# Kernel tuning notes

Hardware: AMD Instinct MI355X
Metric: run time of the kernel (lower is better)

Reference implementation:

```python
import jax, jax.numpy as jnp
import numpy as np

STRIDE = 1
PADDING = 1

def setup_inputs() -> dict:
    key = jax.random.key(0)
    k1, k2, k3 = jax.random.split(key, 3)
    N, C_in, H, W = 32, 128, 56, 56
    C_out, K = 256, 3
    inputs = jax.random.normal(k1, (N, C_in, H, W), dtype=jnp.float32)
    # trunc_normal(std=0.1) approximated by clipped normal
    filters = jnp.clip(jax.random.normal(k2, (C_out, C_in, K, K), dtype=jnp.float32) * 0.1, -0.2, 0.2)
    bias = jnp.clip(jax.random.normal(k3, (C_out,), dtype=jnp.float32) * 0.1, -0.2, 0.2)
    return {"inputs": inputs, "filters": filters, "bias": bias}

def reference(inputs, filters, bias):
    # Equivalent of the quadruple-loop conv: standard cross-correlation,
    # NCHW input, OIHW filters, stride/padding from module config.
    out = jax.lax.conv_general_dilated(
        inputs, filters,
        window_strides=(STRIDE, STRIDE),
        padding=[(PADDING, PADDING), (PADDING, PADDING)],
        dimension_numbers=("NCHW", "OIHW", "NCHW"),
    )
    out = out + bias[None, :, None, None]
    return out
```

## Files before the change

kernel.cpp:

```cpp
#include <hip/hip_runtime.h>

#define CIN    128
#define HH     56
#define WW_    56
#define NBATCH 32
#define COUT   256
#define KTOT   1152
#define PLANE  3136
#define HP     58
#define BM     128
#define BN     128
#define BK     64

#define WB_OFF   0
#define WB_BYTES (COUT * KTOT * 2)
#define XP_OFF   (1u << 20)
#define XP_BYTES (NBATCH * HP * HP * CIN * 2)

typedef __attribute__((ext_vector_type(8))) short bf16x8;
typedef __attribute__((ext_vector_type(4))) float f32x4;

__device__ __forceinline__ unsigned short f2bf(float f) {
    unsigned int u = __builtin_bit_cast(unsigned int, f);
    u += 0x7fffu + ((u >> 16) & 1u);
    return (unsigned short)(u >> 16);
}

__device__ __forceinline__ void gl_lds16(const void* g, void* l) {
    __builtin_amdgcn_global_load_lds(
        (const __attribute__((address_space(1))) void*)g,
        (__attribute__((address_space(3))) void*)l, 16, 0, 0);
}

__global__ void wprep(const float* __restrict__ w, unsigned short* __restrict__ wb) {
    const int o = blockIdx.x;
    const int t = threadIdx.x;
    #pragma unroll
    for (int e = 0; e < 5; ++e) {
        const int k = t + e * 256;
        if (k < KTOT) {
            const int tap = k >> 7;
            const int ci  = k & 127;
            wb[o * KTOT + k] = f2bf(w[(o * CIN + ci) * 9 + tap]);
        }
    }
}

__global__ void xprep(const float* __restrict__ in, unsigned short* __restrict__ xp) {
    const int b = blockIdx.x;
    const int n = b / HH;
    const int h = b - n * HH;
    const int w  = threadIdx.x & 63;
    const int cg = threadIdx.x >> 6;
    if (w >= WW_) return;
    const float* ib = in + ((size_t)n * CIN) * PLANE + h * WW_ + w;
    unsigned short* ob = xp + (((size_t)n * HP + (h + 1)) * HP + (w + 1)) * CIN;
    #pragma unroll
    for (int e = 0; e < 4; ++e) {
        const int chunk = cg + e * 4;
        uint4 pk;
        unsigned v[8];
        #pragma unroll
        for (int i = 0; i < 8; ++i)
            v[i] = f2bf(ib[(size_t)(chunk * 8 + i) * PLANE]);
        pk.x = v[0] | (v[1] << 16);
        pk.y = v[2] | (v[3] << 16);
        pk.z = v[4] | (v[5] << 16);
        pk.w = v[6] | (v[7] << 16);
        *(uint4*)(ob + chunk * 8) = pk;
    }
}

__global__ __launch_bounds__(256, 2)
void conv_mfma(const unsigned short* __restrict__ wb,
               const unsigned short* __restrict__ xp,
               const float* __restrict__ bias,
               float* __restrict__ out)
{
    __shared__ __align__(16) unsigned short Asm_[BM * BK];
    __shared__ __align__(16) unsigned short Bsm_[BN * BK];

    const int t    = threadIdx.x;
    const int pix0 = blockIdx.x * BN;
    const int c0   = blockIdx.y * BM;

    const int slot = t & 7;
    const int r32  = t >> 3;
    const int swiz = (slot ^ (r32 & 7)) * 16;

    const char* aBase = (const char*)wb + (size_t)(c0 + r32) * (KTOT * 2) + swiz;
    const char* bBase[4];
    #pragma unroll
    for (int p = 0; p < 4; ++p) {
        const int pix = pix0 + r32 + p * 32;
        const int n   = pix / PLANE;
        const int rem = pix - n * PLANE;
        const int h   = rem / WW_;
        const int w   = rem - h * WW_;
        bBase[p] = (const char*)xp + ((size_t)(n * HP + h) * HP + w) * (CIN * 2) + swiz;
    }

    const int lane = t & 63;
    const int wave = t >> 6;
    const int wm   = (wave & 1) * 64;
    const int wn   = (wave >> 1) * 64;
    const int lr   = lane & 15;
    const int quad = lane >> 4;
    const int rmod = lr & 7;

    f32x4 acc[4][4];
    #pragma unroll
    for (int i = 0; i < 4; ++i)
        #pragma unroll
        for (int j = 0; j < 4; ++j)
            acc[i][j] = (f32x4){0.f, 0.f, 0.f, 0.f};

    char* const asmb = (char*)Asm_;
    char* const bsmb = (char*)Bsm_;

    for (int tap = 0; tap < 9; ++tap) {
        const int toff = ((tap / 3) * HP + (tap % 3)) * (CIN * 2);
        for (int ci0b = 0; ci0b < 256; ci0b += 128) {
            const int abyte = tap * 256 + ci0b;
            #pragma unroll
            for (int p = 0; p < 4; ++p)
                gl_lds16(aBase + (size_t)p * 32 * (KTOT * 2) + abyte, asmb + p * 4096 + t * 16);
            #pragma unroll
            for (int p = 0; p < 4; ++p)
                gl_lds16(bBase[p] + toff + ci0b, bsmb + p * 4096 + t * 16);
            __syncthreads();

            #pragma unroll
            for (int kk = 0; kk < 2; ++kk) {
                bf16x8 af[4], bfr[4];
                #pragma unroll
                for (int i = 0; i < 4; ++i) {
                    const int r = wm + i * 16 + lr;
                    const int phys = ((kk * 4 + quad) ^ rmod) * 16;
                    af[i] = *(const bf16x8*)(asmb + r * 128 + phys);
                }
                #pragma unroll
                for (int j = 0; j < 4; ++j) {
                    const int r = wn + j * 16 + lr;
                    const int phys = ((kk * 4 + quad) ^ rmod) * 16;
                    bfr[j] = *(const bf16x8*)(bsmb + r * 128 + phys);
                }
                #pragma unroll
                for (int i = 0; i < 4; ++i)
                    #pragma unroll
                    for (int j = 0; j < 4; ++j)
                        acc[i][j] = __builtin_amdgcn_mfma_f32_16x16x32_bf16(af[i], bfr[j], acc[i][j], 0, 0, 0);
            }
            __syncthreads();
        }
    }

    #pragma unroll
    for (int j = 0; j < 4; ++j) {
        const int pg    = pix0 + wn + j * 16 + lr;
        const int ni    = pg / PLANE;
        const int inner = pg - ni * PLANE;
        float* op = out + (size_t)ni * (COUT * PLANE) + inner;
        #pragma unroll
        for (int i = 0; i < 4; ++i) {
            const int crow = c0 + wm + i * 16 + quad * 4;
            #pragma unroll
            for (int r = 0; r < 4; ++r)
                op[(size_t)(crow + r) * PLANE] = acc[i][j][r] + bias[crow + r];
        }
    }
}

extern "C" void kernel_launch(void* const* d_in, const int* in_sizes, int n_in,
                              void* d_out, int out_size, void* d_ws, size_t ws_size,
                              hipStream_t stream) {
    const float* in   = (const float*)d_in[0];
    const float* wt   = (const float*)d_in[1];
    const float* bias = (const float*)d_in[2];
    float* out        = (float*)d_out;

    unsigned short* wb = (unsigned short*)((char*)d_ws + WB_OFF);
    unsigned short* xp = (unsigned short*)((char*)d_ws + XP_OFF);

    hipMemsetAsync(xp, 0, XP_BYTES, stream);
    wprep<<<COUT, 256, 0, stream>>>(wt, wb);
    xprep<<<NBATCH * HH, 256, 0, stream>>>(in, xp);

    dim3 grid((NBATCH * PLANE) / BN, COUT / BM);
    conv_mfma<<<grid, 256, 0, stream>>>(wb, xp, bias, out);
}
```

Baseline: 219.1 us.

## Fuse padding into xprep with LDS transpose; coalesce weight prep reads

The separate memset of the padded input buffer is removed. The input-prep kernel now runs over all 58 padded rows and writes the zero border itself. Each block transposes one input row through shared memory so global reads stay coalesced along width and writes go out as full 16-byte NHWC chunks. The weight-prep kernel now reads the source contiguously and scatters its writes instead. This cuts one full pass over the padded buffer and improves access patterns in the prep stage, at the cost of LDS traffic and bank conflicts in the transpose.

New measurement: 208.9 us. 1.05x faster.

```diff
diff --git a/kernel.cpp b/kernel.cpp
--- a/kernel.cpp
+++ b/kernel.cpp
@@ -13,9 +13,7 @@
 #define BK     64
 
 #define WB_OFF   0
-#define WB_BYTES (COUT * KTOT * 2)
 #define XP_OFF   (1u << 20)
-#define XP_BYTES (NBATCH * HP * HP * CIN * 2)
 
 typedef __attribute__((ext_vector_type(8))) short bf16x8;
 typedef __attribute__((ext_vector_type(4))) float f32x4;
@@ -35,39 +33,70 @@
 __global__ void wprep(const float* __restrict__ w, unsigned short* __restrict__ wb) {
     const int o = blockIdx.x;
     const int t = threadIdx.x;
+    const float* src = w + (size_t)o * KTOT;
+    unsigned short* dst = wb + (size_t)o * KTOT;
     #pragma unroll
     for (int e = 0; e < 5; ++e) {
-        const int k = t + e * 256;
-        if (k < KTOT) {
-            const int tap = k >> 7;
-            const int ci  = k & 127;
-            wb[o * KTOT + k] = f2bf(w[(o * CIN + ci) * 9 + tap]);
-        }
-    }
-}
-
-__global__ void xprep(const float* __restrict__ in, unsigned short* __restrict__ xp) {
-    const int b = blockIdx.x;
-    const int n = b / HH;
-    const int h = b - n * HH;
-    const int w  = threadIdx.x & 63;
-    const int cg = threadIdx.x >> 6;
-    if (w >= WW_) return;
-    const float* ib = in + ((size_t)n * CIN) * PLANE + h * WW_ + w;
-    unsigned short* ob = xp + (((size_t)n * HP + (h + 1)) * HP + (w + 1)) * CIN;
+        const int idx = t + e * 256;
+        if (idx < KTOT) {
+            const int ci  = idx / 9;
+            const int tap = idx - ci * 9;
+            dst[tap * 128 + ci] = f2bf(src[idx]);
+        }
+    }
+}
+
+__global__ __launch_bounds__(256)
+void xprep(const float* __restrict__ in, unsigned short* __restrict__ xp) {
+    const int b  = blockIdx.x;
+    const int n  = b / HP;
+    const int ho = b - n * HP;
+    const int t  = threadIdx.x;
+    uint4* orow = (uint4*)(xp + (((size_t)n * HP + ho) * HP) * CIN);
+
+    if (ho == 0 || ho == HP - 1) {
+        #pragma unroll
+        for (int e = 0; e < 4; ++e) {
+            const int idx = t + e * 256;
+            if (idx < 928) orow[idx] = (uint4){0u, 0u, 0u, 0u};
+        }
+        return;
+    }
+
+    __shared__ unsigned short L[CIN * 57];
+    const int h  = ho - 1;
+    const int w  = t & 63;
+    const int cb = t >> 6;
+    if (w < WW_) {
+        const float* ib = in + ((size_t)n * CIN) * PLANE + (size_t)h * WW_ + w;
+        #pragma unroll
+        for (int e = 0; e < 32; ++e) {
+            const int ci = cb * 32 + e;
+            L[ci * 57 + w] = f2bf(ib[(size_t)ci * PLANE]);
+        }
+    }
+    __syncthreads();
+
     #pragma unroll
     for (int e = 0; e < 4; ++e) {
-        const int chunk = cg + e * 4;
-        uint4 pk;
-        unsigned v[8];
-        #pragma unroll
-        for (int i = 0; i < 8; ++i)
-            v[i] = f2bf(ib[(size_t)(chunk * 8 + i) * PLANE]);
-        pk.x = v[0] | (v[1] << 16);
-        pk.y = v[2] | (v[3] << 16);
-        pk.z = v[4] | (v[5] << 16);
-        pk.w = v[6] | (v[7] << 16);
-        *(uint4*)(ob + chunk * 8) = pk;
+        const int idx = t + e * 256;
+        if (idx < 928) {
+            const int wo = idx >> 4;
+            const int ch = idx & 15;
+            uint4 pk = {0u, 0u, 0u, 0u};
+            if (wo >= 1 && wo <= WW_) {
+                const int wi = wo - 1;
+                unsigned v[8];
+                #pragma unroll
+                for (int i = 0; i < 8; ++i)
+                    v[i] = L[(ch * 8 + i) * 57 + wi];
+                pk.x = v[0] | (v[1] << 16);
+                pk.y = v[2] | (v[3] << 16);
+                pk.z = v[4] | (v[5] << 16);
+                pk.w = v[6] | (v[7] << 16);
+            }
+            orow[idx] = pk;
+        }
     }
 }
 
@@ -182,9 +211,8 @@
     unsigned short* wb = (unsigned short*)((char*)d_ws + WB_OFF);
     unsigned short* xp = (unsigned short*)((char*)d_ws + XP_OFF);
 
-    hipMemsetAsync(xp, 0, XP_BYTES, stream);
     wprep<<<COUT, 256, 0, stream>>>(wt, wb);
-    xprep<<<NBATCH * HH, 256, 0, stream>>>(in, xp);
+    xprep<<<NBATCH * HP, 256, 0, stream>>>(in, xp);
 
     dim3 grid((NBATCH * PLANE) / BN, COUT / BM);
     conv_mfma<<<grid, 256, 0, stream>>>(wb, xp, bias, out);
```
